# Kernel optimization log

Hardware: AMD Instinct MI355X
Metric: run time of the kernel (lower is better)

## Reference

```python
import jax, jax.numpy as jnp
import numpy as np

H = 256       # hidden_size
W2V = 300     # word embedding dim
POS = 30      # pos embedding dim
NF = 100      # filters per n-gram CNN
VOCAB = 50000
NPOS = 100
N_EDUS = 1024
L = 20        # tokens per EDU


def setup_inputs() -> dict:
    key = jax.random.key(0)
    ks = jax.random.split(key, 22)
    def nrm(k, shape, s=0.05):
        return jax.random.normal(k, shape, dtype=jnp.float32) * s
    cw = W2V + POS  # CNN input width = 330
    # valid transition sequence: S, then (S, R) repeated n-1 times -> 2n-1 steps
    transes = jnp.concatenate([jnp.zeros((1,), jnp.int32),
                               jnp.tile(jnp.array([0, 1], jnp.int32), N_EDUS - 1)])
    return {
        "edu_words": jax.random.randint(ks[0], (N_EDUS, L), 0, VOCAB),
        "edu_poses": jax.random.randint(ks[1], (N_EDUS, L), 0, NPOS),
        "transes": transes,
        "word_emb": nrm(ks[2], (VOCAB, W2V), 1.0),
        "pos_emb": nrm(ks[3], (NPOS, POS), 1.0),
        "Wu": nrm(ks[4], (NF, 1, 1, cw)), "bu": nrm(ks[5], (NF,)),
        "Wb": nrm(ks[6], (NF, 1, 2, cw)), "bb": nrm(ks[7], (NF,)),
        "Wt": nrm(ks[8], (NF, 1, 3, cw)), "bt": nrm(ks[9], (NF,)),
        "Wp": nrm(ks[10], (2 * H, 2 * W2V + POS + 3 * NF)), "bp": nrm(ks[11], (2 * H,)),
        "Wih": nrm(ks[12], (4 * H, 3 * H)), "Whh": nrm(ks[13], (4 * H, H)),
        "bih": nrm(ks[14], (4 * H,)), "bhh": nrm(ks[15], (4 * H,)),
        "Wc": nrm(ks[16], (5 * H, 3 * H)), "bc": nrm(ks[17], (5 * H,)),
        "Ws": nrm(ks[18], (2, H)), "bs": nrm(ks[19], (2,)),
    }


def _encode_edus(edu_words, edu_poses, word_emb, pos_emb, Wu, bu, Wb, bb, Wt, bt, Wp, bp):
    we = word_emb[edu_words]                # [N, L, 300]
    pe = pos_emb[edu_poses]                 # [N, L, 30]
    x = jnp.concatenate([we, pe], axis=-1)[:, None, :, :]  # NCHW [N,1,L,330]
    def conv_pool(W, b, pad):
        # kernel spans full width -> output width 1; pad only along time
        y = jax.lax.conv_general_dilated(x, W, (1, 1), ((pad, pad), (0, 0)),
                                         dimension_numbers=("NCHW", "OIHW", "NCHW"))[..., 0]
        return jax.nn.relu(y + b[None, :, None]).max(axis=-1)  # [N, F]
    feats = jnp.concatenate([we[:, 0], we[:, -1], pe[:, 0],
                             conv_pool(Wu, bu, 0), conv_pool(Wb, bb, 1),
                             conv_pool(Wt, bt, 2)], axis=-1)   # [N, 930]
    h, c = jnp.split(feats @ Wp.T + bp, 2, axis=-1)
    return h, c


def _parse_loss(edu_words, edu_poses, transes, word_emb, pos_emb, Wu, bu, Wb, bb, Wt, bt,
                Wp, bp, Wih, Whh, bih, bhh, Wc, bc, Ws, bs):
    eh, ec = _encode_edus(edu_words, edu_poses, word_emb, pos_emb, Wu, bu, Wb, bb, Wt, bt, Wp, bp)
    M = N_EDUS + 2
    buf_h = jnp.concatenate([eh, jnp.zeros((2, H), jnp.float32)], axis=0)
    buf_c = jnp.concatenate([ec, jnp.zeros((2, H), jnp.float32)], axis=0)
    stack_h = jnp.zeros((M, H), jnp.float32)  # slots 0,1 are the initial placeholders
    stack_c = jnp.zeros((M, H), jnp.float32)

    def lstm(xv, h, c):  # torch LSTMCell gate order i,f,g,o
        g = xv @ Wih.T + bih + h @ Whh.T + bhh
        i, f, gg, o = jnp.split(g, 4)
        c2 = jax.nn.sigmoid(f) * c + jax.nn.sigmoid(i) * jnp.tanh(gg)
        return jax.nn.sigmoid(o) * jnp.tanh(c2), c2

    def track(sh, sptr, bptr, th, tc):
        xv = jnp.concatenate([sh[sptr - 1], sh[sptr - 2], buf_h[bptr]])
        return lstm(xv, th, tc)

    sptr = jnp.int32(2)
    bptr = jnp.int32(0)
    th, tc = track(stack_h, sptr, bptr, jnp.zeros(H, jnp.float32), jnp.zeros(H, jnp.float32))

    def step(carry, trans):
        sh, sc, sptr, bptr, th, tc = carry
        logits = th @ Ws.T + bs  # scorer MLP with mlp_layers=1 -> single Linear
        is_shift = trans == 0
        # SHIFT candidate: push buffer front
        sh_s = sh.at[sptr].set(buf_h[bptr])
        sc_s = sc.at[sptr].set(buf_c[bptr])
        # REDUCE candidate: tree-LSTM composition of top two stack items
        h1, c1 = sh[sptr - 1], sc[sptr - 1]
        h2, c2 = sh[sptr - 2], sc[sptr - 2]
        g = jnp.concatenate([h1, h2, th]) @ Wc.T + bc
        a, i, f1, f2, o = jnp.split(g, 5)
        rc = jnp.tanh(a) * jax.nn.sigmoid(i) + jax.nn.sigmoid(f1) * c1 + jax.nn.sigmoid(f2) * c2
        rh = jax.nn.sigmoid(o) * jnp.tanh(rc)
        sh_r = sh.at[sptr - 2].set(rh)
        sc_r = sc.at[sptr - 2].set(rc)
        sh2 = jnp.where(is_shift, sh_s, sh_r)
        sc2 = jnp.where(is_shift, sc_s, sc_r)
        sptr2 = jnp.where(is_shift, sptr + 1, sptr - 1)
        bptr2 = jnp.where(is_shift, bptr + 1, bptr)
        th2, tc2 = track(sh2, sptr2, bptr2, th, tc)
        return (sh2, sc2, sptr2, bptr2, th2, tc2), logits

    _, pred = jax.lax.scan(step, (stack_h, stack_c, sptr, bptr, th, tc), transes)
    logp = jax.nn.log_softmax(pred, axis=-1)
    return -jnp.mean(logp[jnp.arange(transes.shape[0]), transes])


def reference(edu_words, edu_poses, transes, word_emb, pos_emb, Wu, bu, Wb, bb, Wt, bt,
              Wp, bp, Wih, Whh, bih, bhh, Wc, bc, Ws, bs):
    return _parse_loss(edu_words, edu_poses, transes, word_emb, pos_emb, Wu, bu, Wb, bb,
                       Wt, bt, Wp, bp, Wih, Whh, bih, bhh, Wc, bc, Ws, bs)
```

## Files before the change

kernel.cpp:

```cpp
#include <hip/hip_runtime.h>
#include <math.h>

#define NEDU  1024
#define LTOK  20
#define CW    330
#define HDIM  256
#define FEAT  930
#define MSLOT 1026
#define NWG   32
#define JW    8

typedef unsigned long long u64;

#define O_WCATT 0
#define SZ_WCATT (330*600)
#define O_F     (O_WCATT + SZ_WCATT)
#define SZ_F    (NEDU*FEAT)
#define O_BUFH  (O_F + SZ_F)
#define SZ_BUF  (MSLOT*HDIM)
#define O_BUFC  (O_BUFH + SZ_BUF)
#define O_STKT  (O_BUFC + SZ_BUF)
#define O_THT   (O_STKT + MSLOT*HDIM)
#define O_RHT   (O_THT + 2*HDIM)
#define O_LOSSP (O_RHT + HDIM)
#define NZERO   ((MSLOT + 3) * HDIM)

#define AG __HIP_MEMORY_SCOPE_AGENT
__device__ __forceinline__ u64 aload64(const u64* p) {
  return __hip_atomic_load(p, __ATOMIC_RELAXED, AG);
}
__device__ __forceinline__ void astore(unsigned* p, unsigned v) {
  __hip_atomic_store(p, v, __ATOMIC_RELAXED, AG);
}
__device__ __forceinline__ unsigned tagbits(float v, unsigned ver) {
  return (__float_as_uint(v) & ~3u) | (ver & 3u);
}
__device__ __forceinline__ bool tagok(u64 v, unsigned tag) {
  return (((unsigned)v & 3u) == tag) & (((unsigned)(v >> 32) & 3u) == tag);
}
__device__ __forceinline__ float sigm(float x) { return 1.f / (1.f + expf(-x)); }
__device__ __forceinline__ void unpack(u64 a, u64 b, float* x) {
  x[0] = __uint_as_float((unsigned)a); x[1] = __uint_as_float((unsigned)(a >> 32));
  x[2] = __uint_as_float((unsigned)b); x[3] = __uint_as_float((unsigned)(b >> 32));
}
__device__ __forceinline__ void sync_lds() {
  asm volatile("s_waitcnt lgkmcnt(0)\n\ts_barrier" ::: "memory");
}
__device__ __forceinline__ void gather1T(const unsigned* base, int lane, unsigned tag,
                                         float* x) {
  const u64* p = (const u64*)base + 2 * lane;
  for (int it = 0;; ++it) {
    const u64 a = aload64(p), b = aload64(p + 1);
    if (__ballot(tagok(a, tag) & tagok(b, tag)) == ~0ull) { unpack(a, b, x); return; }
    if (it > 48) __builtin_amdgcn_s_sleep(1);
  }
}
__device__ __forceinline__ void gather2T(const unsigned* b1, unsigned t1,
                                         const unsigned* b2, unsigned t2,
                                         int lane, float* x1, float* x2) {
  const u64* p1 = (const u64*)b1 + 2 * lane;
  const u64* p2 = (const u64*)b2 + 2 * lane;
  for (int it = 0;; ++it) {
    const u64 a = aload64(p1), b = aload64(p1 + 1);
    const u64 c = aload64(p2), d = aload64(p2 + 1);
    const bool ok = tagok(a, t1) & tagok(b, t1) & tagok(c, t2) & tagok(d, t2);
    if (__ballot(ok) == ~0ull) { unpack(a, b, x1); unpack(c, d, x2); return; }
    if (it > 48) __builtin_amdgcn_s_sleep(1);
  }
}

__global__ void prep_kernel(const float* __restrict__ Wu, const float* __restrict__ Wb,
                            const float* __restrict__ Wt, float* __restrict__ ws) {
  const int i0 = blockIdx.x * blockDim.x + threadIdx.x;
  const int st = gridDim.x * blockDim.x;
  for (int i = i0; i < SZ_WCATT; i += st) {
    const int k = i / 600, c = i - 600 * k;
    float v;
    if (c < 100)      v = Wu[c * 330 + k];
    else if (c < 300) { const int q = c - 100; v = Wb[(q % 100) * 660 + (q / 100) * 330 + k]; }
    else              { const int q = c - 300; v = Wt[(q % 100) * 990 + (q / 100) * 330 + k]; }
    ws[O_WCATT + i] = v;
  }
  unsigned* z = (unsigned*)ws + O_STKT;
  for (int i = i0; i < NZERO; i += st) z[i] = 0u;
  for (int i = i0; i < 2 * HDIM; i += st) {
    ws[O_BUFH + NEDU * HDIM + i] = 0.f;
    ws[O_BUFC + NEDU * HDIM + i] = 0.f;
  }
}

__global__ __launch_bounds__(256) void encode_kernel(
    const int* __restrict__ edu_words, const int* __restrict__ edu_poses,
    const float* __restrict__ word_emb, const float* __restrict__ pos_emb,
    const float* __restrict__ bu, const float* __restrict__ bb,
    const float* __restrict__ bt, float* __restrict__ ws) {
  __shared__ __align__(16) float xlT[CW * LTOK];
  __shared__ float zl[300 * 21];
  __shared__ float convout[300];
  const int n = blockIdx.x, tid = threadIdx.x;
  const float* WcatT = ws + O_WCATT;

  for (int i = tid; i < LTOK * CW; i += 256) {
    const int l = i / CW, k = i - l * CW;
    float v;
    if (k < 300) v = word_emb[(size_t)edu_words[n * LTOK + l] * 300 + k];
    else         v = pos_emb[(size_t)edu_poses[n * LTOK + l] * 30 + (k - 300)];
    xlT[k * LTOK + l] = v;
  }
  __syncthreads();

  for (int f = tid; f < 300; f += 256) {
    float acc[LTOK];
#pragma unroll
    for (int l = 0; l < LTOK; ++l) acc[l] = 0.f;
    for (int k = 0; k < CW; ++k) {
      const float w = WcatT[k * 600 + f];
      const float4* xp = (const float4*)(xlT + k * LTOK);
      union { float4 v[5]; float s[20]; } xu;
      xu.v[0] = xp[0]; xu.v[1] = xp[1]; xu.v[2] = xp[2]; xu.v[3] = xp[3]; xu.v[4] = xp[4];
#pragma unroll
      for (int l = 0; l < LTOK; ++l) acc[l] += w * xu.s[l];
    }
#pragma unroll
    for (int l = 0; l < LTOK; ++l) zl[f * 21 + l] = acc[l];
  }
  __syncthreads();
  if (tid < 200) {
    float m;
    if (tid < 100) {
      const int f = tid; const float b = bu[f];
      m = zl[f * 21] + b;
      for (int l = 1; l < 20; ++l) m = fmaxf(m, zl[f * 21 + l] + b);
    } else {
      const int f = tid - 100; const float b = bb[f];
      const float* z0 = zl + (100 + f) * 21;
      const float* z1 = zl + (200 + f) * 21;
      m = z1[0] + b;
      for (int u = 1; u <= 19; ++u) m = fmaxf(m, z0[u - 1] + z1[u] + b);
      m = fmaxf(m, z0[19] + b);
    }
    convout[tid] = fmaxf(m, 0.f);
  }
  __syncthreads();

  for (int f = tid; f < 300; f += 256) {
    float acc[LTOK];
#pragma unroll
    for (int l = 0; l < LTOK; ++l) acc[l] = 0.f;
    for (int k = 0; k < CW; ++k) {
      const float w = WcatT[k * 600 + 300 + f];
      const float4* xp = (const float4*)(xlT + k * LTOK);
      union { float4 v[5]; float s[20]; } xu;
      xu.v[0] = xp[0]; xu.v[1] = xp[1]; xu.v[2] = xp[2]; xu.v[3] = xp[3]; xu.v[4] = xp[4];
#pragma unroll
      for (int l = 0; l < LTOK; ++l) acc[l] += w * xu.s[l];
    }
#pragma unroll
    for (int l = 0; l < LTOK; ++l) zl[f * 21 + l] = acc[l];
  }
  __syncthreads();
  if (tid < 100) {
    const int f = tid; const float b = bt[f];
    const float* z0 = zl + f * 21;
    const float* z1 = zl + (100 + f) * 21;
    const float* z2 = zl + (200 + f) * 21;
    float m = z2[0] + b;
    m = fmaxf(m, z1[0] + z2[1] + b);
    for (int u = 2; u <= 19; ++u) m = fmaxf(m, z0[u - 2] + z1[u - 1] + z2[u] + b);
    m = fmaxf(m, z0[18] + z1[19] + b);
    m = fmaxf(m, z0[19] + b);
    convout[200 + f] = fmaxf(m, 0.f);
  }
  __syncthreads();

  float* Fr = ws + O_F + (size_t)n * FEAT;
  for (int j = tid; j < FEAT; j += 256) {
    float v;
    if (j < 300)      v = xlT[j * LTOK + 0];
    else if (j < 600) v = xlT[(j - 300) * LTOK + 19];
    else if (j < 630) v = xlT[(j - 300) * LTOK + 0];
    else              v = convout[j - 630];
    Fr[j] = v;
  }
}

__global__ __launch_bounds__(256) void proj_kernel(const float* __restrict__ Wp,
                                                   const float* __restrict__ bp,
                                                   float* __restrict__ ws) {
  __shared__ float As[64][17];
  __shared__ float Bs[64][17];
  const float* F = ws + O_F;
  float* bufh = ws + O_BUFH;
  float* bufc = ws + O_BUFC;
  const int tid = threadIdx.x;
  const int m0 = blockIdx.x * 64, n0 = blockIdx.y * 64;
  const int mm0 = (tid & 15) * 4, nn0 = (tid >> 4) * 4;
  float acc[4][4] = {{0.f}};
  for (int k0 = 0; k0 < FEAT; k0 += 16) {
    for (int i = tid; i < 64 * 16; i += 256) {
      const int mm = i >> 4, kk = i & 15;
      const int gk = k0 + kk;
      As[mm][kk] = (gk < FEAT) ? F[(size_t)(m0 + mm) * FEAT + gk] : 0.f;
      Bs[mm][kk] = (gk < FEAT) ? Wp[(size_t)(n0 + mm) * FEAT + gk] : 0.f;
    }
    __syncthreads();
#pragma unroll
    for (int kk = 0; kk < 16; ++kk) {
      float av[4], bv[4];
#pragma unroll
      for (int i = 0; i < 4; ++i) av[i] = As[mm0 + i][kk];
#pragma unroll
      for (int j = 0; j < 4; ++j) bv[j] = Bs[nn0 + j][kk];
#pragma unroll
      for (int i = 0; i < 4; ++i)
#pragma unroll
        for (int j = 0; j < 4; ++j) acc[i][j] += av[i] * bv[j];
    }
    __syncthreads();
  }
#pragma unroll
  for (int i = 0; i < 4; ++i) {
    const int m = m0 + mm0 + i;
#pragma unroll
    for (int j = 0; j < 4; ++j) {
      const int nn = n0 + nn0 + j;
      const float v = acc[i][j] + bp[nn];
      if (nn < 256) bufh[(size_t)m * 256 + nn] = v;
      else          bufc[(size_t)m * 256 + (nn - 256)] = v;
    }
  }
}

__global__ __launch_bounds__(256, 1) void parse_kernel(
    const int* __restrict__ transes, int nT,
    const float* __restrict__ Wih, const float* __restrict__ Whh,
    const float* __restrict__ bih, const float* __restrict__ bhh,
    const float* __restrict__ Wc, const float* __restrict__ bc,
    const float* __restrict__ Wsc, float* __restrict__ ws) {
  const int tid = threadIdx.x;
  const int lane = tid & 63;
  const int wv = tid >> 6;
  const int bx = blockIdx.x;
  const int j0 = bx * JW;

  const float* bufh = ws + O_BUFH;
  const float* bufc = ws + O_BUFC;
  unsigned* stkT = (unsigned*)ws + O_STKT;
  unsigned* thT  = (unsigned*)ws + O_THT;
  unsigned* rhT  = (unsigned*)ws + O_RHT;
  float* lossp   = ws + O_LOSSP;

  __shared__ float sc_lds[MSLOT][JW];
  __shared__ unsigned vstk[MSLOT];
  __shared__ float g_lds[5 * JW];
  __shared__ float part_lds[2 * JW];

  float wt[JW][16]; float bt_[JW];
#pragma unroll
  for (int q = 0; q < JW; ++q) {
    const int rg = wv * 256 + j0 + q;
#pragma unroll
    for (int blk = 0; blk < 3; ++blk) {
      const float4 w = *(const float4*)(Wih + (size_t)rg * 768 + blk * 256 + 4 * lane);
      wt[q][4 * blk + 0] = w.x; wt[q][4 * blk + 1] = w.y;
      wt[q][4 * blk + 2] = w.z; wt[q][4 * blk + 3] = w.w;
    }
    const float4 wh = *(const float4*)(Whh + (size_t)rg * 256 + 4 * lane);
    wt[q][12] = wh.x; wt[q][13] = wh.y; wt[q][14] = wh.z; wt[q][15] = wh.w;
    bt_[q] = bih[rg] + bhh[rg];
  }
  float wcm[10][12]; float bc_[10];
#pragma unroll
  for (int q = 0; q < 10; ++q) {
    const int r = 10 * wv + q, gate = r >> 3, jj = r & 7;
    const int rg = gate * 256 + j0 + jj;
#pragma unroll
    for (int blk = 0; blk < 3; ++blk) {
      const float4 w = *(const float4*)(Wc + (size_t)rg * 768 + blk * 256 + 4 * lane);
      wcm[q][4 * blk + 0] = w.x; wcm[q][4 * blk + 1] = w.y;
      wcm[q][4 * blk + 2] = w.z; wcm[q][4 * blk + 3] = w.w;
    }
    bc_[q] = bc[rg];
  }
  float ws0 = 0.f, ws1 = 0.f;
  if (tid < JW) { ws0 = Wsc[j0 + tid]; ws1 = Wsc[256 + j0 + tid]; }

  for (int i = tid; i < MSLOT; i += 256) vstk[i] = 0u;
  if (tid < JW) { sc_lds[0][tid] = 0.f; sc_lds[1][tid] = 0.f; }
  __syncthreads();

  unsigned V = 0, vrh = 0;
  int sptr = 2, bptr = 0;
  float tc_reg = 0.f;
  float rh_reg = 0.f;

  auto red8 = [&](float* d) {
#pragma unroll
    for (int off = 32; off; off >>= 1) {
#pragma unroll
      for (int q = 0; q < 8; ++q) d[q] += __shfl_down(d[q], off, 64);
    }
  };
  auto red10 = [&](float* d) {
#pragma unroll
    for (int off = 32; off; off >>= 1) {
#pragma unroll
      for (int q = 0; q < 10; ++q) d[q] += __shfl_down(d[q], off, 64);
    }
  };

  auto dyn_track = [&](const unsigned* fbase, unsigned ftag, int fblk, float* d) {
    float x[4];
    gather1T(fbase, lane, ftag, x);
#pragma unroll
    for (int q = 0; q < JW; ++q) {
#pragma unroll
      for (int c = 0; c < 4; ++c) d[q] += wt[q][4 * fblk + c] * x[c];
    }
    red8(d);
    if (lane == 0) {
#pragma unroll
      for (int q = 0; q < JW; ++q) g_lds[wv * JW + q] = d[q] + bt_[q];
    }
    sync_lds();
    if (tid < JW) {
      const int j = j0 + tid;
      const float gi = g_lds[tid], gf = g_lds[8 + tid], gg = g_lds[16 + tid],
                  go = g_lds[24 + tid];
      const float cn = sigm(gf) * tc_reg + sigm(gi) * tanhf(gg);
      tc_reg = cn;
      const float th = sigm(go) * tanhf(cn);
      astore(thT + ((V + 1) & 1) * HDIM + j, tagbits(th, V + 1));
      part_lds[tid] = ws0 * th; part_lds[JW + tid] = ws1 * th;
    }
    if (tid == 0) {
      float a0 = 0.f, a1 = 0.f;
#pragma unroll
      for (int q = 0; q < JW; ++q) { a0 += part_lds[q]; a1 += part_lds[JW + q]; }
      float* lp = lossp + (size_t)V * 64 + bx * 2;
      lp[0] = a0; lp[1] = a1;
    }
  };

  auto stat3 = [&](const float* p1, const float* p2, const float* p3, float* d) {
#pragma unroll
    for (int q = 0; q < JW; ++q) {
      float a = 0.f;
#pragma unroll
      for (int c = 0; c < 4; ++c)
        a += wt[q][c] * p1[c] + wt[q][4 + c] * p2[c] + wt[q][8 + c] * p3[c];
      d[q] = a;
    }
  };

  {
    const float4 f3 = *(const float4*)(bufh + 4 * lane);
    float p1[4], p2[4];
    gather2T(stkT + HDIM, 0u, stkT, 0u, lane, p1, p2);
    const float p3[4] = { f3.x, f3.y, f3.z, f3.w };
    float d[JW];
    stat3(p1, p2, p3, d);
    dyn_track(thT, 0u, 3, d);
    sync_lds();
    V += 1;
  }

  for (int t = 0; t < nT; ++t) {
    const int tr = transes[t];
    if (tr) {
      {
        float h1[4], h2[4], xth[4];
        gather2T(stkT + (size_t)(sptr - 1) * HDIM, vstk[sptr - 1] & 3,
                 stkT + (size_t)(sptr - 2) * HDIM, vstk[sptr - 2] & 3, lane, h1, h2);
        float e[10];
#pragma unroll
        for (int q = 0; q < 10; ++q) {
          float a = 0.f;
#pragma unroll
          for (int c = 0; c < 4; ++c)
            a += wcm[q][c] * h1[c] + wcm[q][4 + c] * h2[c];
          e[q] = a;
        }
        gather1T(thT + (V & 1) * HDIM, lane, V & 3, xth);
#pragma unroll
        for (int q = 0; q < 10; ++q) {
#pragma unroll
          for (int c = 0; c < 4; ++c) e[q] += wcm[q][8 + c] * xth[c];
        }
        red10(e);
        if (lane == 0) {
#pragma unroll
          for (int q = 0; q < 10; ++q) g_lds[10 * wv + q] = e[q] + bc_[q];
        }
        sync_lds();
        if (tid < JW) {
          const float ga = g_lds[tid], gi = g_lds[8 + tid], gf1 = g_lds[16 + tid],
                      gf2 = g_lds[24 + tid], go = g_lds[32 + tid];
          const float c1 = sc_lds[sptr - 1][tid];
          const float c2 = sc_lds[sptr - 2][tid];
          const float rc = tanhf(ga) * sigm(gi) + sigm(gf1) * c1 + sigm(gf2) * c2;
          sc_lds[sptr - 2][tid] = rc;
          rh_reg = sigm(go) * tanhf(rc);
          astore(rhT + j0 + tid, tagbits(rh_reg, vrh + 1));
        }
        vrh += 1;
        sync_lds();
      }
      {
        const float4 f3 = *(const float4*)(bufh + (size_t)bptr * HDIM + 4 * lane);
        float p2[4], xth[4];
        gather2T(stkT + (size_t)(sptr - 3) * HDIM, vstk[sptr - 3] & 3,
                 thT + (V & 1) * HDIM, V & 3, lane, p2, xth);
        const float p3[4] = { f3.x, f3.y, f3.z, f3.w };
        float d[JW];
#pragma unroll
        for (int q = 0; q < JW; ++q) {
          float a = 0.f;
#pragma unroll
          for (int c = 0; c < 4; ++c)
            a += wt[q][4 + c] * p2[c] + wt[q][8 + c] * p3[c] + wt[q][12 + c] * xth[c];
          d[q] = a;
        }
        float xr[4];
        gather1T(rhT, lane, vrh & 3, xr);
        const unsigned nv2 = vstk[sptr - 2] + 1;
        if (tid < JW) astore(stkT + (size_t)(sptr - 2) * HDIM + j0 + tid,
                             tagbits(rh_reg, nv2));
#pragma unroll
        for (int q = 0; q < JW; ++q) {
#pragma unroll
          for (int c = 0; c < 4; ++c) d[q] += wt[q][c] * xr[c];
        }
        red8(d);
        if (lane == 0) {
#pragma unroll
          for (int q = 0; q < JW; ++q) g_lds[wv * JW + q] = d[q] + bt_[q];
        }
        sync_lds();
        if (tid < JW) {
          const int j = j0 + tid;
          const float gi = g_lds[tid], gf = g_lds[8 + tid], gg = g_lds[16 + tid],
                      go = g_lds[24 + tid];
          const float cn = sigm(gf) * tc_reg + sigm(gi) * tanhf(gg);
          tc_reg = cn;
          const float th = sigm(go) * tanhf(cn);
          astore(thT + ((V + 1) & 1) * HDIM + j, tagbits(th, V + 1));
          part_lds[tid] = ws0 * th; part_lds[JW + tid] = ws1 * th;
        }
        if (tid == 0) {
          float a0 = 0.f, a1 = 0.f;
#pragma unroll
          for (int q = 0; q < JW; ++q) { a0 += part_lds[q]; a1 += part_lds[JW + q]; }
          float* lp = lossp + (size_t)V * 64 + bx * 2;
          lp[0] = a0; lp[1] = a1;
        }
        if (tid == 0) vstk[sptr - 2] = nv2;
        sync_lds();
        V += 1; sptr -= 1;
      }
    } else {
      const unsigned nv = vstk[sptr] + 1;
      if (tid < JW) {
        const int j = j0 + tid;
        astore(stkT + (size_t)sptr * HDIM + j, tagbits(bufh[(size_t)bptr * HDIM + j], nv));
        sc_lds[sptr][tid] = bufc[(size_t)bptr * HDIM + j];
      }
      const float4 f1 = *(const float4*)(bufh + (size_t)bptr * HDIM + 4 * lane);
      const float4 f3 = *(const float4*)(bufh + (size_t)(bptr + 1) * HDIM + 4 * lane);
      float p2[4];
      gather1T(stkT + (size_t)(sptr - 1) * HDIM, lane, vstk[sptr - 1] & 3, p2);
      const float p1[4] = { f1.x, f1.y, f1.z, f1.w };
      const float p3[4] = { f3.x, f3.y, f3.z, f3.w };
      float d[JW];
      stat3(p1, p2, p3, d);
      dyn_track(thT + (V & 1) * HDIM, V & 3, 3, d);
      if (tid == 0) vstk[sptr] = nv;
      sync_lds();
      V += 1; sptr += 1; bptr += 1;
    }
  }
}

__global__ __launch_bounds__(256) void loss_kernel(const int* __restrict__ transes, int nT,
                                                   const float* __restrict__ bsc,
                                                   const float* __restrict__ ws,
                                                   float* __restrict__ out) {
  const int tid = threadIdx.x;
  const float* lossp = ws + O_LOSSP;
  __shared__ double red[256];
  double acc = 0.0;
  for (int t = tid; t < nT; t += 256) {
    const float* lp = lossp + (size_t)t * 64;
    float a0 = 0.f, a1 = 0.f;
    for (int w = 0; w < NWG; ++w) { a0 += lp[2 * w]; a1 += lp[2 * w + 1]; }
    const float l0 = a0 + bsc[0], l1 = a1 + bsc[1];
    const float mx = fmaxf(l0, l1);
    acc += (double)(mx + logf(expf(l0 - mx) + expf(l1 - mx)) - (transes[t] ? l1 : l0));
  }
  red[tid] = acc;
  __syncthreads();
  for (int s = 128; s; s >>= 1) {
    if (tid < s) red[tid] += red[tid + s];
    __syncthreads();
  }
  if (tid == 0) out[0] = (float)(red[0] / (double)nT);
}

extern "C" void kernel_launch(void* const* d_in, const int* in_sizes, int n_in,
                              void* d_out, int out_size, void* d_ws, size_t ws_size,
                              hipStream_t stream) {
  const int*   edu_words = (const int*)d_in[0];
  const int*   edu_poses = (const int*)d_in[1];
  const int*   transes   = (const int*)d_in[2];
  const float* word_emb  = (const float*)d_in[3];
  const float* pos_emb   = (const float*)d_in[4];
  const float* Wu  = (const float*)d_in[5];
  const float* bu  = (const float*)d_in[6];
  const float* Wb  = (const float*)d_in[7];
  const float* bb  = (const float*)d_in[8];
  const float* Wt  = (const float*)d_in[9];
  const float* bt  = (const float*)d_in[10];
  const float* Wp  = (const float*)d_in[11];
  const float* bp  = (const float*)d_in[12];
  const float* Wih = (const float*)d_in[13];
  const float* Whh = (const float*)d_in[14];
  const float* bih = (const float*)d_in[15];
  const float* bhh = (const float*)d_in[16];
  const float* Wc  = (const float*)d_in[17];
  const float* bc  = (const float*)d_in[18];
  const float* Wsc = (const float*)d_in[19];
  const float* bsc = (const float*)d_in[20];
  float* ws  = (float*)d_ws;
  float* out = (float*)d_out;
  int nT = in_sizes[2];

  hipLaunchKernelGGL(prep_kernel, dim3(256), dim3(256), 0, stream, Wu, Wb, Wt, ws);
  hipLaunchKernelGGL(encode_kernel, dim3(NEDU), dim3(256), 0, stream,
                     edu_words, edu_poses, word_emb, pos_emb, bu, bb, bt, ws);
  hipLaunchKernelGGL(proj_kernel, dim3(16, 8), dim3(256), 0, stream, Wp, bp, ws);

  void* args[] = { (void*)&transes, (void*)&nT, (void*)&Wih, (void*)&Whh, (void*)&bih,
                   (void*)&bhh, (void*)&Wc, (void*)&bc, (void*)&Wsc, (void*)&ws };
  hipLaunchCooperativeKernel((const void*)parse_kernel, dim3(NWG), dim3(256), args, 0, stream);

  hipLaunchKernelGGL(loss_kernel, dim3(1), dim3(256), 0, stream, transes, nT, bsc, ws, out);
}
```

Baseline: 8.655 ms.

## Split parse recurrence across 128 single-wave workgroups to remove intra-block barriers

Reworks the sequential parse kernel from 32 workgroups of 4 waves, each owning 8 hidden units, into 128 workgroups of one wave, each owning 2 hidden units across all gates. Gate reduction and cell updates now happen inside a single wave, so the LDS round-trips and s_barrier syncs at every step go away, and tagged outputs are published with packed 64-bit atomic stores. The loss partials are resized to 128 slots. In exchange, more workgroups take part in each global tag-polling exchange, and each wave holds the full set of gate weights in registers.

```diff
diff --git a/kernel.cpp b/kernel.cpp
--- a/kernel.cpp
+++ b/kernel.cpp
@@ -7,8 +7,7 @@
 #define HDIM  256
 #define FEAT  930
 #define MSLOT 1026
-#define NWG   32
-#define JW    8
+#define NWG   128
 
 typedef unsigned long long u64;
 
@@ -29,7 +28,7 @@
 __device__ __forceinline__ u64 aload64(const u64* p) {
   return __hip_atomic_load(p, __ATOMIC_RELAXED, AG);
 }
-__device__ __forceinline__ void astore(unsigned* p, unsigned v) {
+__device__ __forceinline__ void astore64(u64* p, u64 v) {
   __hip_atomic_store(p, v, __ATOMIC_RELAXED, AG);
 }
 __device__ __forceinline__ unsigned tagbits(float v, unsigned ver) {
@@ -42,9 +41,6 @@
 __device__ __forceinline__ void unpack(u64 a, u64 b, float* x) {
   x[0] = __uint_as_float((unsigned)a); x[1] = __uint_as_float((unsigned)(a >> 32));
   x[2] = __uint_as_float((unsigned)b); x[3] = __uint_as_float((unsigned)(b >> 32));
-}
-__device__ __forceinline__ void sync_lds() {
-  asm volatile("s_waitcnt lgkmcnt(0)\n\ts_barrier" ::: "memory");
 }
 __device__ __forceinline__ void gather1T(const unsigned* base, int lane, unsigned tag,
                                          float* x) {
@@ -231,17 +227,15 @@
   }
 }
 
-__global__ __launch_bounds__(256, 1) void parse_kernel(
+__global__ __launch_bounds__(64, 1) void parse_kernel(
     const int* __restrict__ transes, int nT,
     const float* __restrict__ Wih, const float* __restrict__ Whh,
     const float* __restrict__ bih, const float* __restrict__ bhh,
     const float* __restrict__ Wc, const float* __restrict__ bc,
     const float* __restrict__ Wsc, float* __restrict__ ws) {
-  const int tid = threadIdx.x;
-  const int lane = tid & 63;
-  const int wv = tid >> 6;
+  const int lane = threadIdx.x;
   const int bx = blockIdx.x;
-  const int j0 = bx * JW;
+  const int j0 = bx * 2;
 
   const float* bufh = ws + O_BUFH;
   const float* bufc = ws + O_BUFC;
@@ -250,15 +244,13 @@
   unsigned* rhT  = (unsigned*)ws + O_RHT;
   float* lossp   = ws + O_LOSSP;
 
-  __shared__ float sc_lds[MSLOT][JW];
+  __shared__ float sc_lds[MSLOT][2];
   __shared__ unsigned vstk[MSLOT];
-  __shared__ float g_lds[5 * JW];
-  __shared__ float part_lds[2 * JW];
-
-  float wt[JW][16]; float bt_[JW];
-#pragma unroll
-  for (int q = 0; q < JW; ++q) {
-    const int rg = wv * 256 + j0 + q;
+
+  float wt[8][16]; float bt_[8];
+#pragma unroll
+  for (int q = 0; q < 8; ++q) {
+    const int rg = (q >> 1) * 256 + j0 + (q & 1);
 #pragma unroll
     for (int blk = 0; blk < 3; ++blk) {
       const float4 w = *(const float4*)(Wih + (size_t)rg * 768 + blk * 256 + 4 * lane);
@@ -272,8 +264,7 @@
   float wcm[10][12]; float bc_[10];
 #pragma unroll
   for (int q = 0; q < 10; ++q) {
-    const int r = 10 * wv + q, gate = r >> 3, jj = r & 7;
-    const int rg = gate * 256 + j0 + jj;
+    const int rg = (q >> 1) * 256 + j0 + (q & 1);
 #pragma unroll
     for (int blk = 0; blk < 3; ++blk) {
       const float4 w = *(const float4*)(Wc + (size_t)rg * 768 + blk * 256 + 4 * lane);
@@ -282,17 +273,18 @@
     }
     bc_[q] = bc[rg];
   }
-  float ws0 = 0.f, ws1 = 0.f;
-  if (tid < JW) { ws0 = Wsc[j0 + tid]; ws1 = Wsc[256 + j0 + tid]; }
-
-  for (int i = tid; i < MSLOT; i += 256) vstk[i] = 0u;
-  if (tid < JW) { sc_lds[0][tid] = 0.f; sc_lds[1][tid] = 0.f; }
+  const float ws00 = Wsc[j0], ws01 = Wsc[j0 + 1];
+  const float ws10 = Wsc[256 + j0], ws11 = Wsc[256 + j0 + 1];
+
+  for (int i = lane; i < MSLOT; i += 64) vstk[i] = 0u;
+  if (lane == 0) { sc_lds[0][0] = sc_lds[0][1] = 0.f; sc_lds[1][0] = sc_lds[1][1] = 0.f; }
   __syncthreads();
 
   unsigned V = 0, vrh = 0;
   int sptr = 2, bptr = 0;
-  float tc_reg = 0.f;
-  float rh_reg = 0.f;
+  float tc0 = 0.f, tc1 = 0.f;
+  float rh0 = 0.f, rh1 = 0.f;
+  float xth[4];
 
   auto red8 = [&](float* d) {
 #pragma unroll
@@ -309,42 +301,33 @@
     }
   };
 
-  auto dyn_track = [&](const unsigned* fbase, unsigned ftag, int fblk, float* d) {
-    float x[4];
-    gather1T(fbase, lane, ftag, x);
-#pragma unroll
-    for (int q = 0; q < JW; ++q) {
-#pragma unroll
-      for (int c = 0; c < 4; ++c) d[q] += wt[q][4 * fblk + c] * x[c];
-    }
-    red8(d);
+  auto fin_track = [&](float* d) {
     if (lane == 0) {
-#pragma unroll
-      for (int q = 0; q < JW; ++q) g_lds[wv * JW + q] = d[q] + bt_[q];
-    }
-    sync_lds();
-    if (tid < JW) {
-      const int j = j0 + tid;
-      const float gi = g_lds[tid], gf = g_lds[8 + tid], gg = g_lds[16 + tid],
-                  go = g_lds[24 + tid];
-      const float cn = sigm(gf) * tc_reg + sigm(gi) * tanhf(gg);
-      tc_reg = cn;
-      const float th = sigm(go) * tanhf(cn);
-      astore(thT + ((V + 1) & 1) * HDIM + j, tagbits(th, V + 1));
-      part_lds[tid] = ws0 * th; part_lds[JW + tid] = ws1 * th;
-    }
-    if (tid == 0) {
-      float a0 = 0.f, a1 = 0.f;
-#pragma unroll
-      for (int q = 0; q < JW; ++q) { a0 += part_lds[q]; a1 += part_lds[JW + q]; }
-      float* lp = lossp + (size_t)V * 64 + bx * 2;
-      lp[0] = a0; lp[1] = a1;
-    }
+      float th_[2];
+#pragma unroll
+      for (int jj = 0; jj < 2; ++jj) {
+        const float gi = d[0 + jj] + bt_[0 + jj];
+        const float gf = d[2 + jj] + bt_[2 + jj];
+        const float gg = d[4 + jj] + bt_[4 + jj];
+        const float go = d[6 + jj] + bt_[6 + jj];
+        const float tcp = jj ? tc1 : tc0;
+        const float cn = sigm(gf) * tcp + sigm(gi) * tanhf(gg);
+        if (jj) tc1 = cn; else tc0 = cn;
+        th_[jj] = sigm(go) * tanhf(cn);
+      }
+      const u64 pack = (u64)tagbits(th_[0], V + 1) | ((u64)tagbits(th_[1], V + 1) << 32);
+      astore64((u64*)(thT + ((V + 1) & 1) * HDIM + j0), pack);
+      float2 lp;
+      lp.x = ws00 * th_[0] + ws01 * th_[1];
+      lp.y = ws10 * th_[0] + ws11 * th_[1];
+      *(float2*)(lossp + (size_t)V * 256 + bx * 2) = lp;
+    }
+    V += 1;
   };
 
   auto stat3 = [&](const float* p1, const float* p2, const float* p3, float* d) {
 #pragma unroll
-    for (int q = 0; q < JW; ++q) {
+    for (int q = 0; q < 8; ++q) {
       float a = 0.f;
 #pragma unroll
       for (int c = 0; c < 4; ++c)
@@ -355,21 +338,26 @@
 
   {
     const float4 f3 = *(const float4*)(bufh + 4 * lane);
-    float p1[4], p2[4];
+    float p1[4], p2[4], xf[4];
     gather2T(stkT + HDIM, 0u, stkT, 0u, lane, p1, p2);
     const float p3[4] = { f3.x, f3.y, f3.z, f3.w };
-    float d[JW];
+    float d[8];
     stat3(p1, p2, p3, d);
-    dyn_track(thT, 0u, 3, d);
-    sync_lds();
-    V += 1;
+    gather1T(thT, lane, 0u, xf);
+#pragma unroll
+    for (int q = 0; q < 8; ++q) {
+#pragma unroll
+      for (int c = 0; c < 4; ++c) d[q] += wt[q][12 + c] * xf[c];
+    }
+    red8(d);
+    fin_track(d);
   }
 
   for (int t = 0; t < nT; ++t) {
     const int tr = transes[t];
     if (tr) {
       {
-        float h1[4], h2[4], xth[4];
+        float h1[4], h2[4];
         gather2T(stkT + (size_t)(sptr - 1) * HDIM, vstk[sptr - 1] & 3,
                  stkT + (size_t)(sptr - 2) * HDIM, vstk[sptr - 2] & 3, lane, h1, h2);
         float e[10];
@@ -389,32 +377,34 @@
         }
         red10(e);
         if (lane == 0) {
-#pragma unroll
-          for (int q = 0; q < 10; ++q) g_lds[10 * wv + q] = e[q] + bc_[q];
-        }
-        sync_lds();
-        if (tid < JW) {
-          const float ga = g_lds[tid], gi = g_lds[8 + tid], gf1 = g_lds[16 + tid],
-                      gf2 = g_lds[24 + tid], go = g_lds[32 + tid];
-          const float c1 = sc_lds[sptr - 1][tid];
-          const float c2 = sc_lds[sptr - 2][tid];
-          const float rc = tanhf(ga) * sigm(gi) + sigm(gf1) * c1 + sigm(gf2) * c2;
-          sc_lds[sptr - 2][tid] = rc;
-          rh_reg = sigm(go) * tanhf(rc);
-          astore(rhT + j0 + tid, tagbits(rh_reg, vrh + 1));
+          float rhv[2];
+#pragma unroll
+          for (int jj = 0; jj < 2; ++jj) {
+            const float ga = e[0 + jj] + bc_[0 + jj];
+            const float gi = e[2 + jj] + bc_[2 + jj];
+            const float gf1 = e[4 + jj] + bc_[4 + jj];
+            const float gf2 = e[6 + jj] + bc_[6 + jj];
+            const float go = e[8 + jj] + bc_[8 + jj];
+            const float c1 = sc_lds[sptr - 1][jj];
+            const float c2 = sc_lds[sptr - 2][jj];
+            const float rc = tanhf(ga) * sigm(gi) + sigm(gf1) * c1 + sigm(gf2) * c2;
+            sc_lds[sptr - 2][jj] = rc;
+            rhv[jj] = sigm(go) * tanhf(rc);
+          }
+          rh0 = rhv[0]; rh1 = rhv[1];
+          const u64 pack = (u64)tagbits(rh0, vrh + 1) | ((u64)tagbits(rh1, vrh + 1) << 32);
+          astore64((u64*)(rhT + j0), pack);
         }
         vrh += 1;
-        sync_lds();
       }
       {
         const float4 f3 = *(const float4*)(bufh + (size_t)bptr * HDIM + 4 * lane);
-        float p2[4], xth[4];
-        gather2T(stkT + (size_t)(sptr - 3) * HDIM, vstk[sptr - 3] & 3,
-                 thT + (V & 1) * HDIM, V & 3, lane, p2, xth);
+        float p2[4];
+        gather1T(stkT + (size_t)(sptr - 3) * HDIM, lane, vstk[sptr - 3] & 3, p2);
         const float p3[4] = { f3.x, f3.y, f3.z, f3.w };
-        float d[JW];
-#pragma unroll
-        for (int q = 0; q < JW; ++q) {
+        float d[8];
+#pragma unroll
+        for (int q = 0; q < 8; ++q) {
           float a = 0.f;
 #pragma unroll
           for (int c = 0; c < 4; ++c)
@@ -424,59 +414,48 @@
         float xr[4];
         gather1T(rhT, lane, vrh & 3, xr);
         const unsigned nv2 = vstk[sptr - 2] + 1;
-        if (tid < JW) astore(stkT + (size_t)(sptr - 2) * HDIM + j0 + tid,
-                             tagbits(rh_reg, nv2));
-#pragma unroll
-        for (int q = 0; q < JW; ++q) {
+        if (lane == 0) {
+          const u64 pack = (u64)tagbits(rh0, nv2) | ((u64)tagbits(rh1, nv2) << 32);
+          astore64((u64*)(stkT + (size_t)(sptr - 2) * HDIM + j0), pack);
+          vstk[sptr - 2] = nv2;
+        }
+#pragma unroll
+        for (int q = 0; q < 8; ++q) {
 #pragma unroll
           for (int c = 0; c < 4; ++c) d[q] += wt[q][c] * xr[c];
         }
         red8(d);
-        if (lane == 0) {
-#pragma unroll
-          for (int q = 0; q < JW; ++q) g_lds[wv * JW + q] = d[q] + bt_[q];
-        }
-        sync_lds();
-        if (tid < JW) {
-          const int j = j0 + tid;
-          const float gi = g_lds[tid], gf = g_lds[8 + tid], gg = g_lds[16 + tid],
-                      go = g_lds[24 + tid];
-          const float cn = sigm(gf) * tc_reg + sigm(gi) * tanhf(gg);
-          tc_reg = cn;
-          const float th = sigm(go) * tanhf(cn);
-          astore(thT + ((V + 1) & 1) * HDIM + j, tagbits(th, V + 1));
-          part_lds[tid] = ws0 * th; part_lds[JW + tid] = ws1 * th;
-        }
-        if (tid == 0) {
-          float a0 = 0.f, a1 = 0.f;
-#pragma unroll
-          for (int q = 0; q < JW; ++q) { a0 += part_lds[q]; a1 += part_lds[JW + q]; }
-          float* lp = lossp + (size_t)V * 64 + bx * 2;
-          lp[0] = a0; lp[1] = a1;
-        }
-        if (tid == 0) vstk[sptr - 2] = nv2;
-        sync_lds();
-        V += 1; sptr -= 1;
+        fin_track(d);
+        sptr -= 1;
       }
     } else {
       const unsigned nv = vstk[sptr] + 1;
-      if (tid < JW) {
-        const int j = j0 + tid;
-        astore(stkT + (size_t)sptr * HDIM + j, tagbits(bufh[(size_t)bptr * HDIM + j], nv));
-        sc_lds[sptr][tid] = bufc[(size_t)bptr * HDIM + j];
+      if (lane == 0) {
+        const float b0 = bufh[(size_t)bptr * HDIM + j0];
+        const float b1 = bufh[(size_t)bptr * HDIM + j0 + 1];
+        const u64 pack = (u64)tagbits(b0, nv) | ((u64)tagbits(b1, nv) << 32);
+        astore64((u64*)(stkT + (size_t)sptr * HDIM + j0), pack);
+        sc_lds[sptr][0] = bufc[(size_t)bptr * HDIM + j0];
+        sc_lds[sptr][1] = bufc[(size_t)bptr * HDIM + j0 + 1];
+        vstk[sptr] = nv;
       }
       const float4 f1 = *(const float4*)(bufh + (size_t)bptr * HDIM + 4 * lane);
       const float4 f3 = *(const float4*)(bufh + (size_t)(bptr + 1) * HDIM + 4 * lane);
-      float p2[4];
+      float p2[4], xf[4];
       gather1T(stkT + (size_t)(sptr - 1) * HDIM, lane, vstk[sptr - 1] & 3, p2);
       const float p1[4] = { f1.x, f1.y, f1.z, f1.w };
       const float p3[4] = { f3.x, f3.y, f3.z, f3.w };
-      float d[JW];
+      float d[8];
       stat3(p1, p2, p3, d);
-      dyn_track(thT + (V & 1) * HDIM, V & 3, 3, d);
-      if (tid == 0) vstk[sptr] = nv;
-      sync_lds();
-      V += 1; sptr += 1; bptr += 1;
+      gather1T(thT + (V & 1) * HDIM, lane, V & 3, xf);
+#pragma unroll
+      for (int q = 0; q < 8; ++q) {
+#pragma unroll
+        for (int c = 0; c < 4; ++c) d[q] += wt[q][12 + c] * xf[c];
+      }
+      red8(d);
+      fin_track(d);
+      sptr += 1; bptr += 1;
     }
   }
 }
@@ -490,9 +469,9 @@
   __shared__ double red[256];
   double acc = 0.0;
   for (int t = tid; t < nT; t += 256) {
-    const float* lp = lossp + (size_t)t * 64;
+    const float2* lp = (const float2*)(lossp + (size_t)t * 256);
     float a0 = 0.f, a1 = 0.f;
-    for (int w = 0; w < NWG; ++w) { a0 += lp[2 * w]; a1 += lp[2 * w + 1]; }
+    for (int w = 0; w < NWG; ++w) { const float2 v = lp[w]; a0 += v.x; a1 += v.y; }
     const float l0 = a0 + bsc[0], l1 = a1 + bsc[1];
     const float mx = fmaxf(l0, l1);
     acc += (double)(mx + logf(expf(l0 - mx) + expf(l1 - mx)) - (transes[t] ? l1 : l0));
@@ -541,7 +520,7 @@
 
   void* args[] = { (void*)&transes, (void*)&nT, (void*)&Wih, (void*)&Whh, (void*)&bih,
                    (void*)&bhh, (void*)&Wc, (void*)&bc, (void*)&Wsc, (void*)&ws };
-  hipLaunchCooperativeKernel((const void*)parse_kernel, dim3(NWG), dim3(256), args, 0, stream);
+  hipLaunchCooperativeKernel((const void*)parse_kernel, dim3(NWG), dim3(64), args, 0, stream);
 
   hipLaunchKernelGGL(loss_kernel, dim3(1), dim3(256), 0, stream, transes, nT, bsc, ws, out);
 }
```

New measurement: 8.721 ms. Within noise of the previous version (+0.8%).
